# Kernel optimization log

Measured on AMD Instinct MI355X. Metric: run time of the kernel, lower is better.

## Reference

```python
import jax, jax.numpy as jnp
import numpy as np


def setup_inputs() -> dict:
    key = jax.random.key(0)
    k1, k2 = jax.random.split(key)
    logits = jax.random.normal(k1, (4, 19, 512, 512), dtype=jnp.float32)
    targets = jax.random.randint(k2, (4, 512, 512), 0, 19, dtype=jnp.int64)
    return {"logits": logits, "targets": targets}


def reference(logits, targets):
    # Lovasz-Softmax loss, classes='all', per_image=False, ignore=None.
    B, C, H, W = logits.shape
    probs = jax.nn.softmax(logits, axis=1)                    # [B,C,H,W]
    p = probs.transpose(0, 2, 3, 1).reshape(-1, C)            # [P,C], P=B*H*W
    t = targets.reshape(-1)                                   # [P]
    fg = jax.nn.one_hot(t, C, dtype=p.dtype).T                # [C,P]
    errors = jnp.abs(fg - p.T)                                # [C,P]
    # sort errors descending per class, carry ground-truth along
    perm = jnp.argsort(-errors, axis=1)                       # [C,P]
    errors_sorted = jnp.take_along_axis(errors, perm, axis=1)
    gt_sorted = jnp.take_along_axis(fg, perm, axis=1)
    # Lovasz extension gradient (vectorized over classes)
    gts = gt_sorted.sum(axis=1, keepdims=True)                # [C,1]
    cs = jnp.cumsum(gt_sorted, axis=1)                        # [C,P]
    intersection = gts - cs
    union = gts + jnp.cumsum(1.0 - gt_sorted, axis=1)
    jaccard = 1.0 - intersection / union
    jaccard = jnp.concatenate(
        [jaccard[:, :1], jaccard[:, 1:] - jaccard[:, :-1]], axis=1)
    losses = jnp.sum(errors_sorted * jaccard, axis=1)         # [C]
    return jnp.mean(losses)
```

## Files before the change

kernel.cpp:

```cpp
#include <hip/hip_runtime.h>

constexpr int C    = 19;
constexpr int HW   = 512 * 512;
constexpr int NP   = 4 * HW;
constexpr int NB   = 512;
constexpr int NBLK = 512;
constexpr int TPB  = 1024;
constexpr int PIX_PER_BLK = NP / NBLK;
constexpr int CHUNKS = 16;

__global__ __launch_bounds__(TPB, 8) void lovasz_hist(
    const float* __restrict__ logits,
    const int*   __restrict__ targets,
    unsigned int* __restrict__ partials)
{
    __shared__ unsigned int hist[C * NB];
    const int tid = threadIdx.x;

    for (int i = tid; i < C * NB; i += TPB) hist[i] = 0;
    __syncthreads();

    const int pix = blockIdx.x * PIX_PER_BLK + tid * 2;
    const int b   = pix >> 18;
    const int hw  = pix & (HW - 1);
    const float* lp = logits + (size_t)b * (C * HW) + hw;

    float l[C][2];
#pragma unroll
    for (int c = 0; c < C; ++c) {
        float2 t = *(const float2*)(lp + (size_t)c * HW);
        l[c][0] = t.x; l[c][1] = t.y;
    }
    int t2[2];
    {
        int2 ti = *(const int2*)(targets + pix);
        t2[0] = ti.x; t2[1] = ti.y;
    }

#pragma unroll
    for (int j = 0; j < 2; ++j) {
        float s = 0.f;
#pragma unroll
        for (int c = 0; c < C; ++c) {
            float ex = __expf(l[c][j]);
            l[c][j] = ex;
            s += ex;
        }
        const float inv = 1.0f / s;
        const int   t   = t2[j];
#pragma unroll
        for (int c = 0; c < C; ++c) {
            float p  = l[c][j] * inv;
            bool  fg = (c == t);
            float e  = fg ? 1.0f - p : p;
            int bin = (int)(__fsqrt_rn(e) * (float)NB);
            bin = bin < 0 ? 0 : (bin > NB - 1 ? NB - 1 : bin);
            atomicAdd(&hist[c * NB + bin], fg ? 0x10001u : 1u);
        }
    }

    __syncthreads();
    unsigned int* dst = partials + (size_t)blockIdx.x * (C * NB);
    for (int i = tid; i < C * NB; i += TPB) dst[i] = hist[i];
}

__global__ __launch_bounds__(256) void lovasz_reduce(
    const unsigned int* __restrict__ partials,
    unsigned long long* __restrict__ lvl2,
    float* __restrict__ out)
{
    if (blockIdx.x == 0 && threadIdx.x == 0) out[0] = 0.f;

    const int c   = blockIdx.x / CHUNKS;
    const int ch  = blockIdx.x % CHUNKS;
    const int tid = threadIdx.x;
    const int kpc = NBLK / CHUNKS;

#pragma unroll
    for (int half = 0; half < 2; ++half) {
        const int bin = tid + half * 256;
        unsigned long long acc = 0;
        for (int k = ch * kpc; k < (ch + 1) * kpc; ++k) {
            unsigned v = partials[(size_t)k * (C * NB) + c * NB + bin];
            acc += (unsigned long long)(v & 0xFFFFu) |
                   ((unsigned long long)(v >> 16) << 32);
        }
        lvl2[((size_t)c * CHUNKS + ch) * NB + bin] = acc;
    }
}

__global__ __launch_bounds__(256) void lovasz_loss(
    const unsigned long long* __restrict__ lvl2,
    float* __restrict__ out)
{
    const int c   = blockIdx.x;
    const int tid = threadIdx.x;

    __shared__ unsigned long long sh[NB];
    __shared__ unsigned long long red[256];

    unsigned long long acc0 = 0, acc1 = 0;
#pragma unroll
    for (int ch = 0; ch < CHUNKS; ++ch) {
        const unsigned long long* p = lvl2 + ((size_t)c * CHUNKS + ch) * NB;
        acc0 += p[tid];
        acc1 += p[tid + 256];
    }
    sh[tid]       = acc0;
    sh[tid + 256] = acc1;

    red[tid] = acc0 + acc1;
    __syncthreads();
    for (int off = 128; off > 0; off >>= 1) {
        if (tid < off) red[tid] += red[tid + off];
        __syncthreads();
    }
    const float G = (float)(unsigned)(red[0] >> 32);
    __syncthreads();

    unsigned long long carry = 0;
    float loss = 0.f;
#pragma unroll
    for (int chunk = 0; chunk < NB / 256; ++chunk) {
        const int bin = NB - 1 - (chunk * 256 + tid);
        const unsigned long long v = sh[bin];

        red[tid] = v;
        __syncthreads();
        unsigned long long x = v;
        for (int off = 1; off < 256; off <<= 1) {
            unsigned long long y = (tid >= off) ? red[tid - off] : 0ull;
            __syncthreads();
            x += y;
            red[tid] = x;
            __syncthreads();
        }

        const unsigned long long after  = carry + x;
        const unsigned long long before = after - v;
        if ((unsigned)v) {
            float Ka  = (float)(unsigned)(after);
            float CSa = (float)(unsigned)(after >> 32);
            float Kb  = (float)(unsigned)(before);
            float CSb = (float)(unsigned)(before >> 32);
            float Ja = (Ka > 0.f) ? 1.f - (G - CSa) / (G + Ka - CSa) : 0.f;
            float Jb = (Kb > 0.f) ? 1.f - (G - CSb) / (G + Kb - CSb) : 0.f;
            float r  = ((float)bin + 0.5f) * (1.0f / (float)NB);
            loss += (r * r) * (Ja - Jb);
        }
        carry += red[255];
        __syncthreads();
    }

    __shared__ float sf[256];
    sf[tid] = loss;
    __syncthreads();
    for (int off = 128; off > 0; off >>= 1) {
        if (tid < off) sf[tid] += sf[tid + off];
        __syncthreads();
    }
    if (tid == 0) atomicAdd(out, sf[0] * (1.0f / (float)C));
}

extern "C" void kernel_launch(void* const* d_in, const int* in_sizes, int n_in,
                              void* d_out, int out_size, void* d_ws, size_t ws_size,
                              hipStream_t stream) {
    const float* logits  = (const float*)d_in[0];
    const int*   targets = (const int*)d_in[1];
    float*       out     = (float*)d_out;

    unsigned int*       partials = (unsigned int*)d_ws;
    unsigned long long* lvl2     = (unsigned long long*)
        ((char*)d_ws + (size_t)NBLK * C * NB * sizeof(unsigned int));

    lovasz_hist<<<NBLK, TPB, 0, stream>>>(logits, targets, partials);
    lovasz_reduce<<<C * CHUNKS, 256, 0, stream>>>(partials, lvl2, out);
    lovasz_loss<<<C, 256, 0, stream>>>(lvl2, out);
}
```

Baseline: 130.9 us.

## Process four pixels per thread with two-pass logit reads in histogram kernel

Halves threads per block and gives each thread four pixels loaded as float4. Logits are no longer kept in registers: a first pass accumulates the softmax denominators, and a second pass reloads the logits from global memory, recomputes the exponentials and bins the errors. This trades extra global reads (likely served by cache) and duplicated exp work for lower register pressure and wider vector loads, and it also changes how many atomic updates are in flight per block.

Measured after the change: 176.1 us. 34.5% more time.

```diff
diff --git a/kernel.cpp b/kernel.cpp
--- a/kernel.cpp
+++ b/kernel.cpp
@@ -5,7 +5,7 @@
 constexpr int NP   = 4 * HW;
 constexpr int NB   = 512;
 constexpr int NBLK = 512;
-constexpr int TPB  = 1024;
+constexpr int TPB  = 512;
 constexpr int PIX_PER_BLK = NP / NBLK;
 constexpr int CHUNKS = 16;
 
@@ -20,43 +20,45 @@
     for (int i = tid; i < C * NB; i += TPB) hist[i] = 0;
     __syncthreads();
 
-    const int pix = blockIdx.x * PIX_PER_BLK + tid * 2;
+    const int pix = blockIdx.x * PIX_PER_BLK + tid * 4;
     const int b   = pix >> 18;
     const int hw  = pix & (HW - 1);
     const float* lp = logits + (size_t)b * (C * HW) + hw;
 
-    float l[C][2];
+    float s0 = 0.f, s1 = 0.f, s2 = 0.f, s3 = 0.f;
 #pragma unroll
     for (int c = 0; c < C; ++c) {
-        float2 t = *(const float2*)(lp + (size_t)c * HW);
-        l[c][0] = t.x; l[c][1] = t.y;
+        float4 t = *(const float4*)(lp + (size_t)c * HW);
+        s0 += __expf(t.x); s1 += __expf(t.y);
+        s2 += __expf(t.z); s3 += __expf(t.w);
     }
-    int t2[2];
-    {
-        int2 ti = *(const int2*)(targets + pix);
-        t2[0] = ti.x; t2[1] = ti.y;
-    }
+    const float i0 = 1.f / s0, i1 = 1.f / s1, i2 = 1.f / s2, i3 = 1.f / s3;
+
+    int4 tg = *(const int4*)(targets + pix);
 
 #pragma unroll
-    for (int j = 0; j < 2; ++j) {
-        float s = 0.f;
-#pragma unroll
-        for (int c = 0; c < C; ++c) {
-            float ex = __expf(l[c][j]);
-            l[c][j] = ex;
-            s += ex;
-        }
-        const float inv = 1.0f / s;
-        const int   t   = t2[j];
-#pragma unroll
-        for (int c = 0; c < C; ++c) {
-            float p  = l[c][j] * inv;
-            bool  fg = (c == t);
-            float e  = fg ? 1.0f - p : p;
-            int bin = (int)(__fsqrt_rn(e) * (float)NB);
-            bin = bin < 0 ? 0 : (bin > NB - 1 ? NB - 1 : bin);
-            atomicAdd(&hist[c * NB + bin], fg ? 0x10001u : 1u);
-        }
+    for (int c = 0; c < C; ++c) {
+        float4 t = *(const float4*)(lp + (size_t)c * HW);
+        float p0 = __expf(t.x) * i0;
+        float p1 = __expf(t.y) * i1;
+        float p2 = __expf(t.z) * i2;
+        float p3 = __expf(t.w) * i3;
+        float e0 = (c == tg.x) ? 1.f - p0 : p0;
+        float e1 = (c == tg.y) ? 1.f - p1 : p1;
+        float e2 = (c == tg.z) ? 1.f - p2 : p2;
+        float e3 = (c == tg.w) ? 1.f - p3 : p3;
+        int b0 = (int)(__fsqrt_rn(e0) * (float)NB);
+        int b1 = (int)(__fsqrt_rn(e1) * (float)NB);
+        int b2 = (int)(__fsqrt_rn(e2) * (float)NB);
+        int b3 = (int)(__fsqrt_rn(e3) * (float)NB);
+        b0 = min(max(b0, 0), NB - 1);
+        b1 = min(max(b1, 0), NB - 1);
+        b2 = min(max(b2, 0), NB - 1);
+        b3 = min(max(b3, 0), NB - 1);
+        atomicAdd(&hist[c * NB + b0], (c == tg.x) ? 0x10001u : 1u);
+        atomicAdd(&hist[c * NB + b1], (c == tg.y) ? 0x10001u : 1u);
+        atomicAdd(&hist[c * NB + b2], (c == tg.z) ? 0x10001u : 1u);
+        atomicAdd(&hist[c * NB + b3], (c == tg.w) ? 0x10001u : 1u);
     }
 
     __syncthreads();
```
